# Performance work log

Hardware: AMD Instinct MI355X
Metric: run time of the kernel (lower is better)

Reference implementation:

```python
import jax, jax.numpy as jnp
import numpy as np

N_C = 64
D = 128

def setup_inputs() -> dict:
    key = jax.random.key(0)
    embeddings = jax.random.normal(key, (1024, N_C * D), dtype=jnp.float32)
    return {"embeddings": embeddings}

def reference(embeddings) -> jnp.ndarray:
    two_b, _ = embeddings.shape
    B = two_b // 2
    # (2, B, n_c, d), softmax over last dim
    q = jax.nn.softmax(embeddings.reshape(2, B, N_C, D), axis=-1)
    q_a, q_b = q[0], q[1]  # (B, n_c, d)

    self_sim_loss = -(q_a * q_b).sum() / (B * N_C)

    q_a2 = q_a * q_a
    q_b2 = q_b * q_b
    # Faithful to the repeat/repeat_interleave + bmm: block (i, j) of the
    # (n_c^2, d, d) product equals q2[:, j].T @ q2[:, i]  -> einsum over batch.
    prod_a = jnp.einsum('bjc,bid->ijcd', q_a2, q_a2)  # (n_c, n_c, d, d)
    prod_b = jnp.einsum('bjc,bid->ijcd', q_b2, q_b2)

    # mask out diagonal cluster pairs i == j (done before sqrt in original;
    # entries are strictly positive so masking after sqrt is identical)
    offdiag = (~jnp.eye(N_C, dtype=bool))[:, :, None, None]  # (n_c, n_c, 1, 1)

    raw_a = jnp.where(offdiag, jnp.sqrt(prod_a), 0.0).sum()
    raw_b = jnp.where(offdiag, jnp.sqrt(prod_b), 0.0).sum()

    scale = (N_C * N_C - N_C) * (B ** 0.5)
    cluster_loss = -(raw_a / scale + raw_b / scale) / 2
    return self_sim_loss + cluster_loss
```

## Files before the change

kernel.cpp:

```cpp
#include <hip/hip_runtime.h>
#include <cstdint>
#include <cstddef>

#define NCLUS 64
#define DIM   128
#define BATCH 512
#define QCOLS 8192
#define NPAIR 2016
#define TSTRB (QCOLS * BATCH)
#define FP8SCALE 256.0f

typedef float f32x16 __attribute__((ext_vector_type(16)));
typedef int   i32x4  __attribute__((ext_vector_type(4)));
typedef int   i32x8  __attribute__((ext_vector_type(8)));


__device__ __forceinline__ void ld_lds16(const void* g, void* l) {
  __builtin_amdgcn_global_load_lds(
      (__attribute__((address_space(1))) void*)g,
      (__attribute__((address_space(3))) void*)l, 16, 0, 0);
}

#define FSQRT(x) __builtin_amdgcn_sqrtf(x)

#define VM4_BAR() asm volatile("s_waitcnt vmcnt(4)\n\ts_barrier" ::: "memory")
#define VM0_BAR() asm volatile("s_waitcnt vmcnt(0)\n\ts_barrier" ::: "memory")

__global__ __launch_bounds__(256) void softmax_q2_kernel(
    const float* __restrict__ emb, uint8_t* __restrict__ q2t,
    float* __restrict__ dotPart) {
  __shared__ uint32_t T32[2 * 64 * 33];
  __shared__ float red[4];
  const int c  = blockIdx.y;
  const int bq = blockIdx.x;
  const int tid = threadIdx.x;
  const int w = tid >> 6, lane = tid & 63;
  const int sub = lane >> 5;
  const int col = lane & 31;

  float4 qa = {0.f, 0.f, 0.f, 0.f};
  float dot = 0.f;

#pragma unroll
  for (int k = 0; k < 16; ++k) {
    const int t  = k & 1;
    const int bl = w * 16 + (k >> 1) * 2 + sub;
    const int b  = bq * 64 + bl;
    const float4 v = *(const float4*)(emb +
        ((size_t)(t * BATCH + b) * QCOLS + (size_t)c * DIM + col * 4));

    float mx = fmaxf(fmaxf(v.x, v.y), fmaxf(v.z, v.w));
#pragma unroll
    for (int off = 1; off < 32; off <<= 1) mx = fmaxf(mx, __shfl_xor(mx, off));
    float e0 = __expf(v.x - mx), e1 = __expf(v.y - mx);
    float e2 = __expf(v.z - mx), e3 = __expf(v.w - mx);
    float s = (e0 + e1) + (e2 + e3);
#pragma unroll
    for (int off = 1; off < 32; off <<= 1) s += __shfl_xor(s, off);
    const float inv = 1.0f / s;
    const float q0 = e0 * inv, q1 = e1 * inv, q2 = e2 * inv, q3 = e3 * inv;

    if (t == 0) { qa.x = q0; qa.y = q1; qa.z = q2; qa.w = q3; }
    else        { dot += qa.x * q0 + qa.y * q1 + qa.z * q2 + qa.w * q3; }

    int pk = __builtin_amdgcn_cvt_pk_fp8_f32(q0 * q0 * FP8SCALE,
                                             q1 * q1 * FP8SCALE, 0, false);
    pk = __builtin_amdgcn_cvt_pk_fp8_f32(q2 * q2 * FP8SCALE,
                                         q3 * q3 * FP8SCALE, pk, true);
    T32[(t * 64 + bl) * 33 + col] = (uint32_t)pk;
  }
  __syncthreads();

#pragma unroll
  for (int it = 0; it < 4; ++it) {
    int ch = it * 256 + tid;
    int t = ch >> 9, d = (ch >> 2) & 127, b16 = ch & 3;
    const int dq = d >> 2, sh = (d & 3) * 8;
    uint32_t w0 = 0, w1 = 0, w2 = 0, w3 = 0;
#pragma unroll
    for (int r = 0; r < 4; ++r) {
      w0 |= ((T32[(t * 64 + b16 * 16 +  0 + r) * 33 + dq] >> sh) & 0xFFu) << (8 * r);
      w1 |= ((T32[(t * 64 + b16 * 16 +  4 + r) * 33 + dq] >> sh) & 0xFFu) << (8 * r);
      w2 |= ((T32[(t * 64 + b16 * 16 +  8 + r) * 33 + dq] >> sh) & 0xFFu) << (8 * r);
      w3 |= ((T32[(t * 64 + b16 * 16 + 12 + r) * 33 + dq] >> sh) & 0xFFu) << (8 * r);
    }
    size_t off = (size_t)t * TSTRB + (size_t)(c * DIM + d) * BATCH +
                 (size_t)bq * 64 + b16 * 16;
    uint4 o; o.x = w0; o.y = w1; o.z = w2; o.w = w3;
    *(uint4*)(q2t + off) = o;
  }

#pragma unroll
  for (int off = 1; off < 64; off <<= 1) dot += __shfl_xor(dot, off);
  if (lane == 0) red[w] = dot;
  __syncthreads();
  if (tid == 0) dotPart[blockIdx.y * 8 + blockIdx.x] = red[0] + red[1] + red[2] + red[3];
}

__global__ __launch_bounds__(256) void gram_sqrt_kernel(
    const uint8_t* __restrict__ q2t, float* __restrict__ Spart) {
  __shared__ uint8_t L[3 * 16384 + 16];

  int sidx = ((int)blockIdx.x & 7) * 252 + ((int)blockIdx.x >> 3);
  int q = sidx, gi = 0;
  while (q >= 64 * gi + 28) { q -= 64 * gi + 28; ++gi; }
  int I, J;
  if (q < 64 * gi) {
    int gj = q >> 6, r = q & 63;
    I = gi * 8 + (r >> 3);
    J = gj * 8 + (r & 7);
  } else {
    int dq = q - 64 * gi;
    int il = 1;
    while (il * (il + 1) / 2 <= dq) ++il;
    I = gi * 8 + il;
    J = gi * 8 + (dq - il * (il - 1) / 2);
  }

  const uint8_t* baseA = q2t + (size_t)J * (DIM * BATCH);
  const uint8_t* baseB = q2t + (size_t)I * (DIM * BATCH);

  const int tid  = threadIdx.x;
  const int lane = tid & 63, w = tid >> 6;
  const int wm = w & 1, wn = w >> 1;

  const int t0 = tid, t1 = 256 + tid;
  const int r0s = t0 >> 2, r1s = t1 >> 2;
  const int rot0 = (r0s + (r0s >> 2)) & 3;
  const int rot1 = (r1s + (r1s >> 2)) & 3;
  const int c0s = ((t0 & 3) - rot0) & 3;
  const int c1s = ((t1 & 3) - rot1) & 3;
  const size_t g0 = (size_t)r0s * BATCH + c0s * 16;
  const size_t g1 = (size_t)r1s * BATCH + c1s * 16;
  uint8_t* Lb = L;
  const int ldsw = w * 1024;

  const int h = lane >> 5, r31 = lane & 31;
  const int rot = (r31 + (r31 >> 2)) & 3;
  const int ro1 = ((2 * h + rot) & 3) * 16;
  const int ro2 = ((2 * h + 1 + rot) & 3) * 16;
  const int ArowO = (wm * 64 + r31) * 64;
  const int BrowO = 8192 + (wn * 64 + r31) * 64;

  f32x16 acc[2][2];
#pragma unroll
  for (int i = 0; i < 2; ++i)
#pragma unroll
    for (int j = 0; j < 2; ++j) acc[i][j] = (f32x16)(0.f);

  float S0 = 0.f, S1 = 0.f;

#define CHOFF64(i) ((size_t)((i) >> 3) * TSTRB + (size_t)((i) & 7) * 64)
#define STAGE(bufb, ck) do {                                       \
    ld_lds16(baseA + (ck) + g0, Lb + (bufb) + ldsw);               \
    ld_lds16(baseA + (ck) + g1, Lb + (bufb) + 4096 + ldsw);        \
    ld_lds16(baseB + (ck) + g0, Lb + (bufb) + 8192 + ldsw);        \
    ld_lds16(baseB + (ck) + g1, Lb + (bufb) + 12288 + ldsw);       \
  } while (0)
#define MFMA(a, b, c) __builtin_amdgcn_mfma_scale_f32_32x32x64_f8f6f4(        \
    (a), (b), (c), 0, 0, 0, 0x7F7F7F7F, 0, 0x7F7F7F7F)

  STAGE(0, CHOFF64(0));
  STAGE(16384, CHOFF64(1));

#pragma unroll
  for (int m = 0; m < 16; ++m) {
    if (m < 15) VM4_BAR(); else VM0_BAR();

    if (m < 14) STAGE(((m + 2) % 3) * 16384, CHOFF64(m + 2));

    const int be = (m % 3) * 16384;
    i32x4 alo[2], ahi[2], blo[2], bhi[2];
#pragma unroll
    for (int g = 0; g < 2; ++g) {
      alo[g] = *(const i32x4*)(Lb + be + ArowO + g * 2048 + ro1);
      ahi[g] = *(const i32x4*)(Lb + be + ArowO + g * 2048 + ro2);
      blo[g] = *(const i32x4*)(Lb + be + BrowO + g * 2048 + ro1);
      bhi[g] = *(const i32x4*)(Lb + be + BrowO + g * 2048 + ro2);
    }
    i32x8 af[2], bf[2];
#pragma unroll
    for (int g = 0; g < 2; ++g) {
      af[g] = (i32x8){alo[g].x, alo[g].y, alo[g].z, alo[g].w,
                      ahi[g].x, ahi[g].y, ahi[g].z, ahi[g].w};
      bf[g] = (i32x8){blo[g].x, blo[g].y, blo[g].z, blo[g].w,
                      bhi[g].x, bhi[g].y, bhi[g].z, bhi[g].w};
    }
    __builtin_amdgcn_s_setprio(1);
#pragma unroll
    for (int i = 0; i < 2; ++i)
#pragma unroll
      for (int j = 0; j < 2; ++j)
        acc[i][j] = MFMA(af[i], bf[j], acc[i][j]);
    __builtin_amdgcn_s_setprio(0);

    if (m == 7) {
      float p0 = 0.f, p1 = 0.f, p2 = 0.f, p3 = 0.f;
#pragma unroll
      for (int i = 0; i < 2; ++i)
#pragma unroll
        for (int j = 0; j < 2; ++j) {
#pragma unroll
          for (int e = 0; e < 16; e += 4) {
            p0 += FSQRT(acc[i][j][e    ]);
            p1 += FSQRT(acc[i][j][e + 1]);
            p2 += FSQRT(acc[i][j][e + 2]);
            p3 += FSQRT(acc[i][j][e + 3]);
          }
          acc[i][j] = (f32x16)(0.f);
        }
      S0 = (p0 + p1) + (p2 + p3);
    }
  }

  {
    float p0 = 0.f, p1 = 0.f, p2 = 0.f, p3 = 0.f;
#pragma unroll
    for (int i = 0; i < 2; ++i)
#pragma unroll
      for (int j = 0; j < 2; ++j)
#pragma unroll
        for (int e = 0; e < 16; e += 4) {
          p0 += FSQRT(acc[i][j][e    ]);
          p1 += FSQRT(acc[i][j][e + 1]);
          p2 += FSQRT(acc[i][j][e + 2]);
          p3 += FSQRT(acc[i][j][e + 3]);
        }
    S1 = (p0 + p1) + (p2 + p3);
  }

  float local = (S0 + S1) * (1.0f / 256.0f);
#pragma unroll
  for (int off = 1; off < 64; off <<= 1) local += __shfl_xor(local, off);
  float* fred = (float*)(L + 3 * 16384);
  if (lane == 0) fred[w] = local;
  __syncthreads();
  if (tid == 0) Spart[blockIdx.x] = fred[0] + fred[1] + fred[2] + fred[3];
}

__global__ __launch_bounds__(256) void finalize_kernel(
    const float* __restrict__ P, float* __restrict__ out) {
  __shared__ float rd[8];
  const int tid = threadIdx.x;
  float d = 0.f, s = 0.f;
  for (int i = tid; i < 512; i += 256) d += P[i];
  for (int i = tid; i < NPAIR; i += 256) s += P[512 + i];
#pragma unroll
  for (int off = 1; off < 64; off <<= 1) { d += __shfl_xor(d, off); s += __shfl_xor(s, off); }
  const int w = tid >> 6;
  if ((tid & 63) == 0) { rd[w] = d; rd[4 + w] = s; }
  __syncthreads();
  if (tid == 0) {
    float dt = rd[0] + rd[1] + rd[2] + rd[3];
    float st = rd[4] + rd[5] + rd[6] + rd[7];
    out[0] = -dt / 32768.0f - st / (4032.0f * 22.62741699796952f);
  }
}

extern "C" void kernel_launch(void* const* d_in, const int* in_sizes, int n_in,
                              void* d_out, int out_size, void* d_ws, size_t ws_size,
                              hipStream_t stream) {
  const float* emb = (const float*)d_in[0];
  float* out = (float*)d_out;
  float* P = (float*)d_ws;
  uint8_t* q2t = (uint8_t*)d_ws + 16384;

  softmax_q2_kernel<<<dim3(8, 64), 256, 0, stream>>>(emb, q2t, P);
  gram_sqrt_kernel<<<dim3(NPAIR), 256, 0, stream>>>(q2t, P + 512);
  finalize_kernel<<<1, 256, 0, stream>>>(P, out);
}
```

Baseline: 113.7 us.

## Pair two cluster-pair tiles per block to reuse the A operand

Each gram block now processes one J cluster against two I clusters (I1, I2), so the A-side tile is loaded once and reused across two products. This halves the block count and cuts A-operand global traffic. LDS per stage grows from 16 KB to 24 KB and each wave holds 8 accumulators instead of 4, which raises register and LDS pressure and may lower occupancy. When an odd leftover pair exists, half the waves sit idle.

```diff
diff --git a/kernel.cpp b/kernel.cpp
--- a/kernel.cpp
+++ b/kernel.cpp
@@ -6,7 +6,7 @@
 #define DIM   128
 #define BATCH 512
 #define QCOLS 8192
-#define NPAIR 2016
+#define NBLK2 1024
 #define TSTRB (QCOLS * BATCH)
 #define FP8SCALE 256.0f
 
@@ -23,7 +23,7 @@
 
 #define FSQRT(x) __builtin_amdgcn_sqrtf(x)
 
-#define VM4_BAR() asm volatile("s_waitcnt vmcnt(4)\n\ts_barrier" ::: "memory")
+#define VM6_BAR() asm volatile("s_waitcnt vmcnt(6)\n\ts_barrier" ::: "memory")
 #define VM0_BAR() asm volatile("s_waitcnt vmcnt(0)\n\ts_barrier" ::: "memory")
 
 __global__ __launch_bounds__(256) void softmax_q2_kernel(
@@ -99,39 +99,28 @@
 
 __global__ __launch_bounds__(256) void gram_sqrt_kernel(
     const uint8_t* __restrict__ q2t, float* __restrict__ Spart) {
-  __shared__ uint8_t L[3 * 16384 + 16];
-
-  int sidx = ((int)blockIdx.x & 7) * 252 + ((int)blockIdx.x >> 3);
-  int q = sidx, gi = 0;
-  while (q >= 64 * gi + 28) { q -= 64 * gi + 28; ++gi; }
-  int I, J;
-  if (q < 64 * gi) {
-    int gj = q >> 6, r = q & 63;
-    I = gi * 8 + (r >> 3);
-    J = gj * 8 + (r & 7);
-  } else {
-    int dq = q - 64 * gi;
-    int il = 1;
-    while (il * (il + 1) / 2 <= dq) ++il;
-    I = gi * 8 + il;
-    J = gi * 8 + (dq - il * (il - 1) / 2);
-  }
-
-  const uint8_t* baseA = q2t + (size_t)J * (DIM * BATCH);
-  const uint8_t* baseB = q2t + (size_t)I * (DIM * BATCH);
+  __shared__ uint8_t L[3 * 24576 + 32];
+
+  int sidx = ((int)blockIdx.x & 7) * 128 + ((int)blockIdx.x >> 3);
+  int q = sidx, J = 0;
+  while (q >= ((64 - J) >> 1)) { q -= (64 - J) >> 1; ++J; }
+  const int I1 = J + 1 + 2 * q;
+  const int I2 = I1 + 1;
+  const bool single = (I2 > 63);
+
+  const uint8_t* baseA  = q2t + (size_t)J * (DIM * BATCH);
+  const uint8_t* baseB1 = q2t + (size_t)I1 * (DIM * BATCH);
+  const uint8_t* baseB2 = q2t + (size_t)(single ? I1 : I2) * (DIM * BATCH);
 
   const int tid  = threadIdx.x;
   const int lane = tid & 63, w = tid >> 6;
-  const int wm = w & 1, wn = w >> 1;
-
-  const int t0 = tid, t1 = 256 + tid;
-  const int r0s = t0 >> 2, r1s = t1 >> 2;
-  const int rot0 = (r0s + (r0s >> 2)) & 3;
-  const int rot1 = (r1s + (r1s >> 2)) & 3;
-  const int c0s = ((t0 & 3) - rot0) & 3;
-  const int c1s = ((t1 & 3) - rot1) & 3;
-  const size_t g0 = (size_t)r0s * BATCH + c0s * 16;
-  const size_t g1 = (size_t)r1s * BATCH + c1s * 16;
+  const int wm = w & 1, pr = w >> 1;
+
+  const int rs   = tid >> 2;
+  const int rotS = (rs + (rs >> 2)) & 3;
+  const int cs   = ((tid & 3) - rotS) & 3;
+  const size_t g0 = (size_t)rs * BATCH + cs * 16;
+  const size_t g1 = (size_t)(rs + 64) * BATCH + cs * 16;
   uint8_t* Lb = L;
   const int ldsw = w * 1024;
 
@@ -139,86 +128,94 @@
   const int rot = (r31 + (r31 >> 2)) & 3;
   const int ro1 = ((2 * h + rot) & 3) * 16;
   const int ro2 = ((2 * h + 1 + rot) & 3) * 16;
-  const int ArowO = (wm * 64 + r31) * 64;
-  const int BrowO = 8192 + (wn * 64 + r31) * 64;
-
-  f32x16 acc[2][2];
+  const int ArO = (wm * 64 + r31) * 64;
+  const int BrO = 8192 + pr * 8192 + r31 * 64;
+
+  const bool take = !(single && pr == 1);
+
+  f32x16 acc[2][4];
 #pragma unroll
   for (int i = 0; i < 2; ++i)
 #pragma unroll
-    for (int j = 0; j < 2; ++j) acc[i][j] = (f32x16)(0.f);
+    for (int j = 0; j < 4; ++j) acc[i][j] = (f32x16)(0.f);
 
   float S0 = 0.f, S1 = 0.f;
 
 #define CHOFF64(i) ((size_t)((i) >> 3) * TSTRB + (size_t)((i) & 7) * 64)
-#define STAGE(bufb, ck) do {                                       \
-    ld_lds16(baseA + (ck) + g0, Lb + (bufb) + ldsw);               \
-    ld_lds16(baseA + (ck) + g1, Lb + (bufb) + 4096 + ldsw);        \
-    ld_lds16(baseB + (ck) + g0, Lb + (bufb) + 8192 + ldsw);        \
-    ld_lds16(baseB + (ck) + g1, Lb + (bufb) + 12288 + ldsw);       \
+#define STAGE(bufb, ck) do {                                        \
+    ld_lds16(baseA  + (ck) + g0, Lb + (bufb)         + ldsw);       \
+    ld_lds16(baseA  + (ck) + g1, Lb + (bufb) +  4096 + ldsw);       \
+    ld_lds16(baseB1 + (ck) + g0, Lb + (bufb) +  8192 + ldsw);       \
+    ld_lds16(baseB1 + (ck) + g1, Lb + (bufb) + 12288 + ldsw);       \
+    ld_lds16(baseB2 + (ck) + g0, Lb + (bufb) + 16384 + ldsw);       \
+    ld_lds16(baseB2 + (ck) + g1, Lb + (bufb) + 20480 + ldsw);       \
   } while (0)
 #define MFMA(a, b, c) __builtin_amdgcn_mfma_scale_f32_32x32x64_f8f6f4(        \
     (a), (b), (c), 0, 0, 0, 0x7F7F7F7F, 0, 0x7F7F7F7F)
+#define CAT8(lo, hi) __builtin_shufflevector((lo), (hi), 0, 1, 2, 3, 4, 5, 6, 7)
 
   STAGE(0, CHOFF64(0));
-  STAGE(16384, CHOFF64(1));
+  STAGE(24576, CHOFF64(1));
 
 #pragma unroll
   for (int m = 0; m < 16; ++m) {
-    if (m < 15) VM4_BAR(); else VM0_BAR();
-
-    if (m < 14) STAGE(((m + 2) % 3) * 16384, CHOFF64(m + 2));
-
-    const int be = (m % 3) * 16384;
-    i32x4 alo[2], ahi[2], blo[2], bhi[2];
-#pragma unroll
-    for (int g = 0; g < 2; ++g) {
-      alo[g] = *(const i32x4*)(Lb + be + ArowO + g * 2048 + ro1);
-      ahi[g] = *(const i32x4*)(Lb + be + ArowO + g * 2048 + ro2);
-      blo[g] = *(const i32x4*)(Lb + be + BrowO + g * 2048 + ro1);
-      bhi[g] = *(const i32x4*)(Lb + be + BrowO + g * 2048 + ro2);
+    if (m < 15) VM6_BAR(); else VM0_BAR();
+
+    if (m < 14) STAGE(((m + 2) % 3) * 24576, CHOFF64(m + 2));
+
+    if (take) {
+      const int be = (m % 3) * 24576;
+      i32x8 af[2], bf[4];
+#pragma unroll
+      for (int g = 0; g < 2; ++g) {
+        i32x4 lo = *(const i32x4*)(Lb + be + ArO + g * 2048 + ro1);
+        i32x4 hi = *(const i32x4*)(Lb + be + ArO + g * 2048 + ro2);
+        af[g] = CAT8(lo, hi);
+      }
+#pragma unroll
+      for (int c = 0; c < 4; ++c) {
+        i32x4 lo = *(const i32x4*)(Lb + be + BrO + c * 2048 + ro1);
+        i32x4 hi = *(const i32x4*)(Lb + be + BrO + c * 2048 + ro2);
+        bf[c] = CAT8(lo, hi);
+      }
+      __builtin_amdgcn_s_setprio(1);
+#pragma unroll
+      for (int g = 0; g < 2; ++g)
+#pragma unroll
+        for (int c = 0; c < 4; ++c)
+          acc[g][c] = MFMA(af[g], bf[c], acc[g][c]);
+      __builtin_amdgcn_s_setprio(0);
     }
-    i32x8 af[2], bf[2];
-#pragma unroll
-    for (int g = 0; g < 2; ++g) {
-      af[g] = (i32x8){alo[g].x, alo[g].y, alo[g].z, alo[g].w,
-                      ahi[g].x, ahi[g].y, ahi[g].z, ahi[g].w};
-      bf[g] = (i32x8){blo[g].x, blo[g].y, blo[g].z, blo[g].w,
-                      bhi[g].x, bhi[g].y, bhi[g].z, bhi[g].w};
+
+    if (m == 7) {
+      if (take) {
+        float p0 = 0.f, p1 = 0.f, p2 = 0.f, p3 = 0.f;
+#pragma unroll
+        for (int i = 0; i < 2; ++i)
+#pragma unroll
+          for (int j = 0; j < 4; ++j)
+#pragma unroll
+            for (int e = 0; e < 16; e += 4) {
+              p0 += FSQRT(acc[i][j][e    ]);
+              p1 += FSQRT(acc[i][j][e + 1]);
+              p2 += FSQRT(acc[i][j][e + 2]);
+              p3 += FSQRT(acc[i][j][e + 3]);
+            }
+        S0 = (p0 + p1) + (p2 + p3);
+      }
+#pragma unroll
+      for (int i = 0; i < 2; ++i)
+#pragma unroll
+        for (int j = 0; j < 4; ++j) acc[i][j] = (f32x16)(0.f);
     }
-    __builtin_amdgcn_s_setprio(1);
+  }
+
+  if (take) {
+    float p0 = 0.f, p1 = 0.f, p2 = 0.f, p3 = 0.f;
 #pragma unroll
     for (int i = 0; i < 2; ++i)
 #pragma unroll
-      for (int j = 0; j < 2; ++j)
-        acc[i][j] = MFMA(af[i], bf[j], acc[i][j]);
-    __builtin_amdgcn_s_setprio(0);
-
-    if (m == 7) {
-      float p0 = 0.f, p1 = 0.f, p2 = 0.f, p3 = 0.f;
-#pragma unroll
-      for (int i = 0; i < 2; ++i)
-#pragma unroll
-        for (int j = 0; j < 2; ++j) {
-#pragma unroll
-          for (int e = 0; e < 16; e += 4) {
-            p0 += FSQRT(acc[i][j][e    ]);
-            p1 += FSQRT(acc[i][j][e + 1]);
-            p2 += FSQRT(acc[i][j][e + 2]);
-            p3 += FSQRT(acc[i][j][e + 3]);
-          }
-          acc[i][j] = (f32x16)(0.f);
-        }
-      S0 = (p0 + p1) + (p2 + p3);
-    }
-  }
-
-  {
-    float p0 = 0.f, p1 = 0.f, p2 = 0.f, p3 = 0.f;
-#pragma unroll
-    for (int i = 0; i < 2; ++i)
-#pragma unroll
-      for (int j = 0; j < 2; ++j)
+      for (int j = 0; j < 4; ++j)
 #pragma unroll
         for (int e = 0; e < 16; e += 4) {
           p0 += FSQRT(acc[i][j][e    ]);
@@ -232,7 +229,7 @@
   float local = (S0 + S1) * (1.0f / 256.0f);
 #pragma unroll
   for (int off = 1; off < 64; off <<= 1) local += __shfl_xor(local, off);
-  float* fred = (float*)(L + 3 * 16384);
+  float* fred = (float*)(L + 3 * 24576);
   if (lane == 0) fred[w] = local;
   __syncthreads();
   if (tid == 0) Spart[blockIdx.x] = fred[0] + fred[1] + fred[2] + fred[3];
@@ -244,7 +241,7 @@
   const int tid = threadIdx.x;
   float d = 0.f, s = 0.f;
   for (int i = tid; i < 512; i += 256) d += P[i];
-  for (int i = tid; i < NPAIR; i += 256) s += P[512 + i];
+  for (int i = tid; i < NBLK2; i += 256) s += P[512 + i];
 #pragma unroll
   for (int off = 1; off < 64; off <<= 1) { d += __shfl_xor(d, off); s += __shfl_xor(s, off); }
   const int w = tid >> 6;
@@ -266,6 +263,6 @@
   uint8_t* q2t = (uint8_t*)d_ws + 16384;
 
   softmax_q2_kernel<<<dim3(8, 64), 256, 0, stream>>>(emb, q2t, P);
-  gram_sqrt_kernel<<<dim3(NPAIR), 256, 0, stream>>>(q2t, P + 512);
+  gram_sqrt_kernel<<<dim3(NBLK2), 256, 0, stream>>>(q2t, P + 512);
   finalize_kernel<<<1, 256, 0, stream>>>(P, out);
 }
```

Result: no change. 114.8 us (+1.0%).
